# Kernel optimization log

Hardware: AMD Instinct MI355X
Metric: run time of the kernel (lower is better)

Reference implementation:

```python
import jax, jax.numpy as jnp
import numpy as np

T_SCALE = 160
NUM_SAMPLE = 32
FEAT_DIM = 2048
HIDDEN = 512
N_CLASS = 20
BATCH = 8


def build_sample_mask(tscale=T_SCALE, ns=NUM_SAMPLE):
    # Vectorized version of _get_interp1d_mask (prop_boundary_ratio=0, num_sample_perbin=1).
    # Returns mask of shape [tscale, ns, start, end] (already transposed as in the torch code).
    s = np.arange(tscale)[:, None, None]           # start
    e = np.arange(tscale)[None, :, None]           # end
    k = np.arange(ns)[None, None, :]
    pos = s + (e - s) * k / (ns - 1.0)             # [T, T, ns] sample positions
    Sg, Eg, Kg = np.broadcast_arrays(s, e, k)
    posf = pos.ravel(); Sf = Sg.ravel(); Ef = Eg.ravel(); Kf = Kg.ravel()
    valid = Ef >= Sf
    frac, dn = np.modf(posf)
    dn = dn.astype(np.int64)
    up = np.ceil(posf).astype(np.int64)
    mask = np.zeros((tscale, ns, tscale, tscale), dtype=np.float32)
    m1 = valid & (dn >= 0) & (dn <= tscale - 1)
    np.add.at(mask, (dn[m1], Kf[m1], Sf[m1], Ef[m1]), (1.0 - frac[m1]).astype(np.float32))
    m2 = valid & (up >= 0) & (up <= tscale - 1)
    np.add.at(mask, (up[m2], Kf[m2], Sf[m2], Ef[m2]), frac[m2].astype(np.float32))
    return jnp.asarray(mask)


def conv1d(x, w, padding):
    # x: [B, Cin, T], w: [Cout, Cin, K]
    return jax.lax.conv_general_dilated(
        x, w, window_strides=(1,), padding=[(padding, padding)],
        dimension_numbers=("NCH", "OIH", "NCH"))


def setup_inputs() -> dict:
    key = jax.random.key(0)
    ks = jax.random.split(key, 6)
    x = jax.random.normal(ks[0], (BATCH, T_SCALE, FEAT_DIM), dtype=jnp.float32)
    w1 = jax.random.normal(ks[1], (HIDDEN, FEAT_DIM, 3), dtype=jnp.float32) * 0.02
    b1 = jnp.zeros((HIDDEN,), dtype=jnp.float32)
    wc = jax.random.normal(ks[2], (N_CLASS, HIDDEN, 1), dtype=jnp.float32) * 0.05
    wa = jax.random.normal(ks[3], (1, HIDDEN, 3), dtype=jnp.float32) * 0.05
    ba = jnp.zeros((1,), dtype=jnp.float32)
    sample_mask = build_sample_mask()  # [T, ns, T, T]
    return {"x": x, "sample_mask": sample_mask, "w1": w1, "b1": b1,
            "wc": wc, "wa": wa, "ba": ba}


def reference(x, sample_mask, w1, b1, wc, wa, ba):
    ns = NUM_SAMPLE
    q = ns // 4  # 8
    xp = jnp.transpose(x, (0, 2, 1))                   # [B, F, T]
    feat = jax.nn.relu(conv1d(xp, w1, 1) + b1[None, :, None])   # [B, H, T] (dropout = eval/identity)
    y_class = conv1d(feat, wc, 0)                      # [B, C, T]
    y_atn = conv1d(feat, wa, 1) + ba[None, :, None]    # [B, 1, T]
    # boundary matching: matmul against sparse interpolation mask
    out = jnp.einsum("bct,tkij->bckij", y_class, sample_mask)   # [B, C, ns, T, T]
    out_start = out[:, :, :q].mean(axis=2)
    out_mid = out[:, :, q:ns - q].mean(axis=2)
    out_end = out[:, :, ns - q:].mean(axis=2)
    bmn_class = jnp.concatenate((out_start, out_mid, out_end), axis=1)  # [B, 3C, T, T]
    sig = jax.nn.sigmoid(y_atn)
    x_fg = (sig * feat).sum(-1, keepdims=True) / (sig.sum(-1, keepdims=True) + 1e-8)  # [B, H, 1]
    y_fg = jnp.einsum("oh,bht->bot", wc[:, :, 0], x_fg)  # conv_class 1x1, no bias
    return (y_class, y_fg, bmn_class)
```

## Files before the change

### kernel.cpp

```cpp
#include <hip/hip_runtime.h>
#include <math.h>

#define TS 160
#define FEATD 2048
#define HID 512
#define NC 20
#define NB 8
#define KZ 16

typedef __attribute__((ext_vector_type(8))) short bfrag;
typedef __attribute__((ext_vector_type(4))) float f32x4;

static __device__ __forceinline__ unsigned short f2bf(float f) {
  unsigned int u = __float_as_uint(f);
  unsigned int r = (u + 0x7FFFu + ((u >> 16) & 1u)) >> 16;
  return (unsigned short)r;
}
static __device__ __forceinline__ float bf2f(unsigned short s) {
  return __uint_as_float(((unsigned int)s) << 16);
}

static __device__ __forceinline__ void gload16(const void* g, void* l) {
  __builtin_amdgcn_global_load_lds((const __attribute__((address_space(1))) void*)g,
                                   (__attribute__((address_space(3))) void*)l, 16, 0, 0);
}

__global__ __launch_bounds__(256) void k_prep(const float* __restrict__ x,
                                              const float* __restrict__ w1,
                                              const float* __restrict__ ba,
                                              unsigned short* __restrict__ xb,
                                              unsigned short* __restrict__ wb,
                                              unsigned short* __restrict__ WT,
                                              float* __restrict__ y_atn) {
  __shared__ float Ls[FEATD * 3];
  const int tid = threadIdx.x;
  const int bx = blockIdx.x;
  if (bx < 1296) {
    const int idx = bx * 256 + tid;
    const int c = (idx & 255) * 8;
    const int row = idx >> 8;
    const int b = row / 162, pr = row - b * 162;
    unsigned short* o = xb + (size_t)row * FEATD + c;
    if (pr == 0 || pr == 161) {
      *(uint4*)o = make_uint4(0u, 0u, 0u, 0u);
    } else {
      const float* src = x + ((size_t)(b * TS + pr - 1)) * FEATD + c;
      float4 v0 = *(const float4*)src;
      float4 v1 = *(const float4*)(src + 4);
      unsigned short r[8] = {f2bf(v0.x), f2bf(v0.y), f2bf(v0.z), f2bf(v0.w),
                             f2bf(v1.x), f2bf(v1.y), f2bf(v1.z), f2bf(v1.w)};
      *(uint4*)o = *(const uint4*)r;
    }
  } else if (bx < 1808) {
    const int h = bx - 1296;
    const float4* src = (const float4*)(w1 + (size_t)h * (FEATD * 3));
    for (int e = tid; e < FEATD * 3 / 4; e += 256) ((float4*)Ls)[e] = src[e];
    __syncthreads();
    for (int oc = tid; oc < 768; oc += 256) {
      const int tap = oc >> 8;
      const int f0 = (oc & 255) * 8;
      unsigned short r[8];
      #pragma unroll
      for (int i = 0; i < 8; ++i) r[i] = f2bf(Ls[(f0 + i) * 3 + tap]);
      *(uint4*)&wb[((size_t)tap * HID + h) * FEATD + f0] = *(const uint4*)r;
    }
  } else if (bx < 2408) {
    const int idx = (bx - 1808) * 256 + tid;
    const int tau = idx % 160;
    const int dd = (idx / 160) % 320;
    const int g = idx / (160 * 320);
    float w = 0.f;
    if (dd >= 160) {
      const int d = dd - 160;
      const int k0 = (g == 0) ? 0 : (g == 1 ? 8 : 24);
      const int k1 = (g == 0) ? 8 : (g == 1 ? 24 : 32);
      for (int k = k0; k < k1; ++k) {
        float p = (float)(d * k) / 31.0f;
        float a = fabsf(p - (float)tau);
        w += fmaxf(0.f, 1.f - a);
      }
      w *= (g == 1) ? 0.0625f : 0.125f;
    }
    WT[idx] = f2bf(w);
  } else {
    const int idx = (bx - 2408) * 256 + tid;
    if (idx < NB * TS) y_atn[idx] = ba[0];
  }
}

__global__ __launch_bounds__(256, 2) void k_conv_mfma(const unsigned short* __restrict__ xb,
                                                      const unsigned short* __restrict__ wb,
                                                      unsigned short* __restrict__ part) {
  const int bb = blockIdx.x;
  const int hq = blockIdx.y;
  const int kz = blockIdx.z;
  const int tid = threadIdx.x;
  const int wid = tid >> 6, lane = tid & 63;

  __shared__ unsigned short Alds[162 * 64];
  __shared__ unsigned short Blds[3 * 128 * 64];

  const unsigned short* xbb = xb + (size_t)bb * 162 * FEATD;

  f32x4 acc[5][4] = {};
  const int wr = wid >> 1, wc = wid & 1;

  for (int s = 0; s < 2; ++s) {
    const int f0 = kz * 128 + s * 64;
    #pragma unroll
    for (int is = 0; is < 5; ++is) {
      const int ci = is * 256 + wid * 64 + lane;
      const int row = ci >> 3, c = ci & 7;
      gload16(xbb + (size_t)row * FEATD + f0 + ((c ^ (row & 7)) << 3),
              (char*)Alds + (size_t)(is * 256 + wid * 64) * 16);
    }
    #pragma unroll
    for (int is = 0; is < 12; ++is) {
      const int ci = is * 256 + wid * 64 + lane;
      const int tap = ci >> 10, rr = (ci >> 3) & 127, c = ci & 7;
      gload16(wb + ((size_t)(tap * HID + hq * 128 + rr)) * FEATD + f0 + ((c ^ (rr & 7)) << 3),
              (char*)Blds + (size_t)(is * 256 + wid * 64) * 16);
    }
    if (tid < 16) {
      const int row = 160 + (tid >> 3), c = tid & 7;
      uint4 v = *(const uint4*)(xbb + (size_t)row * FEATD + f0 + ((c ^ (row & 7)) << 3));
      *(uint4*)((char*)Alds + row * 128 + c * 16) = v;
    }
    __syncthreads();

    #pragma unroll
    for (int tap = 0; tap < 3; ++tap) {
      #pragma unroll
      for (int kk = 0; kk < 2; ++kk) {
        const int cc = kk * 4 + (lane >> 4);
        bfrag bfr[4];
        #pragma unroll
        for (int nf = 0; nf < 4; ++nf) {
          const int hh = wc * 64 + nf * 16 + (lane & 15);
          bfr[nf] = *(const bfrag*)((char*)Blds + (size_t)(((tap * 128 + hh) * 8) + (cc ^ (hh & 7))) * 16);
        }
        #pragma unroll
        for (int mi = 0; mi < 5; ++mi) {
          const int rr = wr * 80 + mi * 16 + (lane & 15) + tap;
          bfrag af = *(const bfrag*)((char*)Alds + (size_t)((rr * 8) + (cc ^ (rr & 7))) * 16);
          #pragma unroll
          for (int nf = 0; nf < 4; ++nf)
            acc[mi][nf] = __builtin_amdgcn_mfma_f32_16x16x32_bf16(af, bfr[nf], acc[mi][nf], 0, 0, 0);
        }
      }
    }
    __syncthreads();
  }

  unsigned short* pout = part + (size_t)kz * (NB * TS) * HID;
  #pragma unroll
  for (int mi = 0; mi < 5; ++mi) {
    const int r0 = bb * TS + wr * 80 + mi * 16 + (lane >> 4) * 4;
    #pragma unroll
    for (int nf = 0; nf < 4; ++nf) {
      const int c0 = hq * 128 + wc * 64 + nf * 16 + (lane & 15);
      #pragma unroll
      for (int i = 0; i < 4; ++i)
        pout[(size_t)(r0 + i) * HID + c0] = f2bf(acc[mi][nf][i]);
    }
  }
}

__global__ __launch_bounds__(256) void k_feat_head(const unsigned short* __restrict__ part,
                                                   const float* __restrict__ b1,
                                                   const float* __restrict__ wc,
                                                   const float* __restrict__ wa,
                                                   float* __restrict__ feat,
                                                   float* __restrict__ y_class,
                                                   float* __restrict__ y_atn) {
  const int bt = blockIdx.x;
  const int tid = threadIdx.x;
  __shared__ float fr[HID];
  __shared__ float sred[4][3];
  const int h0 = tid * 2;
  float a0 = b1[h0], a1 = b1[h0 + 1];
  #pragma unroll
  for (int kz = 0; kz < KZ; ++kz) {
    unsigned int v = *(const unsigned int*)&part[(size_t)kz * (NB * TS * HID) + (size_t)bt * HID + h0];
    a0 += bf2f((unsigned short)(v & 0xffff));
    a1 += bf2f((unsigned short)(v >> 16));
  }
  a0 = fmaxf(a0, 0.f);
  a1 = fmaxf(a1, 0.f);
  float2 fo; fo.x = a0; fo.y = a1;
  *(float2*)&feat[(size_t)bt * HID + h0] = fo;
  fr[h0] = a0; fr[h0 + 1] = a1;
  float s0 = a0 * wa[h0 * 3 + 0] + a1 * wa[h0 * 3 + 3];
  float s1 = a0 * wa[h0 * 3 + 1] + a1 * wa[h0 * 3 + 4];
  float s2 = a0 * wa[h0 * 3 + 2] + a1 * wa[h0 * 3 + 5];
  #pragma unroll
  for (int off = 32; off; off >>= 1) {
    s0 += __shfl_xor(s0, off);
    s1 += __shfl_xor(s1, off);
    s2 += __shfl_xor(s2, off);
  }
  const int wv = tid >> 6, lane = tid & 63;
  if (lane == 0) { sred[wv][0] = s0; sred[wv][1] = s1; sred[wv][2] = s2; }
  __syncthreads();
  const int b = bt / TS, t = bt - b * TS;
  for (int c = wv; c < NC; c += 4) {
    float p = 0.f;
    #pragma unroll
    for (int i2 = 0; i2 < 8; ++i2) p += fr[lane + 64 * i2] * wc[c * HID + lane + 64 * i2];
    #pragma unroll
    for (int off = 32; off; off >>= 1) p += __shfl_xor(p, off);
    if (lane == 0) y_class[((size_t)b * NC + c) * TS + t] = p;
  }
  if (tid == 0) {
    float S0 = sred[0][0] + sred[1][0] + sred[2][0] + sred[3][0];
    float S1 = sred[0][1] + sred[1][1] + sred[2][1] + sred[3][1];
    float S2 = sred[0][2] + sred[1][2] + sred[2][2] + sred[3][2];
    atomicAdd(&y_atn[bt], S1);
    if (t < TS - 1) atomicAdd(&y_atn[bt + 1], S0);
    if (t > 0)      atomicAdd(&y_atn[bt - 1], S2);
  }
}

__global__ __launch_bounds__(256) void k_tail(const float* __restrict__ y_class,
                                              const unsigned short* __restrict__ WT,
                                              const float* __restrict__ feat,
                                              const float* __restrict__ y_atn,
                                              const float* __restrict__ wc,
                                              float* __restrict__ y_fg,
                                              float* __restrict__ bmn) {
  __shared__ char Tlds[64000 + 65536];
  const int tid = threadIdx.x;

  if (blockIdx.y == 3) {
    if (blockIdx.x >= NB) return;
    const int b = blockIdx.x;
    float* sig = (float*)Tlds;
    float* red = sig + TS;
    float* xfg = red + 8;
    float s = 0.f;
    if (tid < TS) { s = 1.f / (1.f + expf(-y_atn[b * TS + tid])); sig[tid] = s; }
    float r = s;
    #pragma unroll
    for (int off = 32; off; off >>= 1) r += __shfl_xor(r, off);
    if ((tid & 63) == 0) red[tid >> 6] = r;
    __syncthreads();
    const float inv = 1.f / (red[0] + red[1] + red[2] + red[3] + 1e-8f);
    for (int h = tid; h < HID; h += 256) {
      float a = 0.f;
      for (int t = 0; t < TS; ++t) a += sig[t] * feat[((size_t)b * TS + t) * HID + h];
      xfg[h] = a * inv;
    }
    __syncthreads();
    const int wv = tid >> 6, lane = tid & 63;
    for (int c = wv; c < NC; c += 4) {
      float p = 0.f;
      #pragma unroll
      for (int i2 = 0; i2 < 8; ++i2) {
        int h = lane + 64 * i2;
        p += wc[c * HID + h] * xfg[h];
      }
      #pragma unroll
      for (int off = 32; off; off >>= 1) p += __shfl_xor(p, off);
      if (lane == 0) y_fg[b * NC + c] = p;
    }
    return;
  }

  char* Alds = Tlds;
  char* Wlds = Tlds + 64000;
  const int i = blockIdx.x;
  const int g = blockIdx.y;
  const int wid = tid >> 6, lane = tid & 63;

  const char* wtb = (const char*)WT + (size_t)g * 102400 + (size_t)(160 - i) * 320;
  #pragma unroll
  for (int it = 0; it < 16; ++it) {
    const int idx = it * 256 + tid;
    int row = idx / 25, c = idx - row * 25;
    if (row > 159) row = 159;
    if (c > 19) c = 0;
    gload16(wtb + (size_t)row * 320 + c * 16, Wlds + (size_t)idx * 16);
  }
  for (int e = 0; e < 13; ++e) {
    const int ci = e * 256 + tid;
    if (ci < 3200) {
      const int row = ci / 20, c = ci - row * 20;
      const int tb = i + c * 8;
      const float* yr = y_class + (size_t)row * TS;
      unsigned short r8[8];
      #pragma unroll
      for (int k = 0; k < 8; ++k) {
        const int t = tb + k;
        r8[k] = (t < TS) ? f2bf(yr[t]) : (unsigned short)0;
      }
      *(uint4*)(Alds + (size_t)row * 400 + c * 16) = *(const uint4*)r8;
    }
  }
  __syncthreads();

  const int wr = wid >> 1, wcq = wid & 1;
  f32x4 acc[5][5] = {};

  #pragma unroll
  for (int ks = 0; ks < 5; ++ks) {
    const int cc = ks * 4 + (lane >> 4);
    bfrag bfr[5];
    #pragma unroll
    for (int nf = 0; nf < 5; ++nf) {
      const int j = wcq * 80 + nf * 16 + (lane & 15);
      bfr[nf] = *(const bfrag*)(Wlds + (size_t)j * 400 + cc * 16);
    }
    #pragma unroll
    for (int mf = 0; mf < 5; ++mf) {
      const int r = wr * 80 + mf * 16 + (lane & 15);
      bfrag af = *(const bfrag*)(Alds + (size_t)r * 400 + cc * 16);
      #pragma unroll
      for (int nf = 0; nf < 5; ++nf)
        acc[mf][nf] = __builtin_amdgcn_mfma_f32_16x16x32_bf16(af, bfr[nf], acc[mf][nf], 0, 0, 0);
    }
  }

  #pragma unroll
  for (int mf = 0; mf < 5; ++mf) {
    const int r0 = wr * 80 + mf * 16 + (lane >> 4) * 4;
    #pragma unroll
    for (int reg = 0; reg < 4; ++reg) {
      const int r = r0 + reg;
      const int b = r / 20, c = r - b * 20;
      float* base = bmn + (((size_t)(b * 60 + g * 20 + c) * TS) + i) * TS;
      #pragma unroll
      for (int nf = 0; nf < 5; ++nf) {
        const int j = wcq * 80 + nf * 16 + (lane & 15);
        base[j] = acc[mf][nf][reg];
      }
    }
  }
}

extern "C" void kernel_launch(void* const* d_in, const int* in_sizes, int n_in,
                              void* d_out, int out_size, void* d_ws, size_t ws_size,
                              hipStream_t stream) {
  const float* x  = (const float*)d_in[0];
  const float* w1 = (const float*)d_in[2];
  const float* b1 = (const float*)d_in[3];
  const float* wc = (const float*)d_in[4];
  const float* wa = (const float*)d_in[5];
  const float* ba = (const float*)d_in[6];

  float* out     = (float*)d_out;
  float* y_class = out;
  float* y_fg    = out + NB * NC * TS;
  float* bmn     = out + NB * NC * TS + NB * NC;

  unsigned short* part = (unsigned short*)d_ws;
  float* feat  = (float*)((char*)d_ws + (size_t)KZ * NB * TS * HID * 2);
  float* y_atn = feat + NB * TS * HID;
  unsigned short* xb = (unsigned short*)(y_atn + 2048);
  unsigned short* wb = xb + (size_t)NB * 162 * FEATD;
  unsigned short* WT = wb + (size_t)3 * HID * FEATD;

  k_prep<<<2413, 256, 0, stream>>>(x, w1, ba, xb, wb, WT, y_atn);
  k_conv_mfma<<<dim3(8, 4, KZ), 256, 0, stream>>>(xb, wb, part);
  k_feat_head<<<NB * TS, 256, 0, stream>>>(part, b1, wc, wa, feat, y_class, y_atn);
  k_tail<<<dim3(160, 4), 256, 0, stream>>>(y_class, WT, feat, y_atn, wc, y_fg, bmn);
}
```

Before: 72.38 us.

## Double-buffer conv LDS stages, halve split-K, batch feat_head rows per block

The conv kernel now splits K over 8 chunks instead of 16, so each block handles 256 features in four 64-wide stages. Those stages are double-buffered in LDS so the next stage's global-to-LDS loads are issued while the current one runs MFMAs. The A-tile padding rows are loaded by clamping the row index instead of a separate scalar path. The feat_head kernel processes 4 time rows per block, which reuses the bias and wa loads and cuts the partial-sum reads by half. The trade-off is twice the LDS per conv block, occupancy dropping to one block per CU, and 256 conv blocks where there were 512.

```diff
diff --git a/kernel.cpp b/kernel.cpp
--- a/kernel.cpp
+++ b/kernel.cpp
@@ -6,7 +6,7 @@
 #define HID 512
 #define NC 20
 #define NB 8
-#define KZ 16
+#define KZ 8
 
 typedef __attribute__((ext_vector_type(8))) short bfrag;
 typedef __attribute__((ext_vector_type(4))) float f32x4;
@@ -88,7 +88,7 @@
   }
 }
 
-__global__ __launch_bounds__(256, 2) void k_conv_mfma(const unsigned short* __restrict__ xb,
+__global__ __launch_bounds__(256, 1) void k_conv_mfma(const unsigned short* __restrict__ xb,
                                                       const unsigned short* __restrict__ wb,
                                                       unsigned short* __restrict__ part) {
   const int bb = blockIdx.x;
@@ -97,37 +97,40 @@
   const int tid = threadIdx.x;
   const int wid = tid >> 6, lane = tid & 63;
 
-  __shared__ unsigned short Alds[162 * 64];
-  __shared__ unsigned short Blds[3 * 128 * 64];
+  __shared__ unsigned short Alds[2][12288];
+  __shared__ unsigned short Blds[2][24576];
 
   const unsigned short* xbb = xb + (size_t)bb * 162 * FEATD;
 
   f32x4 acc[5][4] = {};
   const int wr = wid >> 1, wc = wid & 1;
 
-  for (int s = 0; s < 2; ++s) {
-    const int f0 = kz * 128 + s * 64;
-    #pragma unroll
-    for (int is = 0; is < 5; ++is) {
+  auto STAGE = [&](int half, int s) {
+    const int f0 = kz * 256 + s * 64;
+    #pragma unroll
+    for (int is = 0; is < 6; ++is) {
       const int ci = is * 256 + wid * 64 + lane;
-      const int row = ci >> 3, c = ci & 7;
+      int row = ci >> 3;
+      if (row > 161) row = 161;
+      const int c = ci & 7;
       gload16(xbb + (size_t)row * FEATD + f0 + ((c ^ (row & 7)) << 3),
-              (char*)Alds + (size_t)(is * 256 + wid * 64) * 16);
+              (char*)Alds[half] + (size_t)(is * 256 + wid * 64) * 16);
     }
     #pragma unroll
     for (int is = 0; is < 12; ++is) {
       const int ci = is * 256 + wid * 64 + lane;
       const int tap = ci >> 10, rr = (ci >> 3) & 127, c = ci & 7;
       gload16(wb + ((size_t)(tap * HID + hq * 128 + rr)) * FEATD + f0 + ((c ^ (rr & 7)) << 3),
-              (char*)Blds + (size_t)(is * 256 + wid * 64) * 16);
-    }
-    if (tid < 16) {
-      const int row = 160 + (tid >> 3), c = tid & 7;
-      uint4 v = *(const uint4*)(xbb + (size_t)row * FEATD + f0 + ((c ^ (row & 7)) << 3));
-      *(uint4*)((char*)Alds + row * 128 + c * 16) = v;
-    }
-    __syncthreads();
-
+              (char*)Blds[half] + (size_t)(is * 256 + wid * 64) * 16);
+    }
+  };
+
+  STAGE(0, 0);
+  __syncthreads();
+
+  int cur = 0;
+  for (int s = 0; s < 4; ++s) {
+    if (s < 3) STAGE(cur ^ 1, s + 1);
     #pragma unroll
     for (int tap = 0; tap < 3; ++tap) {
       #pragma unroll
@@ -137,12 +140,12 @@
         #pragma unroll
         for (int nf = 0; nf < 4; ++nf) {
           const int hh = wc * 64 + nf * 16 + (lane & 15);
-          bfr[nf] = *(const bfrag*)((char*)Blds + (size_t)(((tap * 128 + hh) * 8) + (cc ^ (hh & 7))) * 16);
+          bfr[nf] = *(const bfrag*)((char*)Blds[cur] + (size_t)(((tap * 128 + hh) * 8) + (cc ^ (hh & 7))) * 16);
         }
         #pragma unroll
         for (int mi = 0; mi < 5; ++mi) {
           const int rr = wr * 80 + mi * 16 + (lane & 15) + tap;
-          bfrag af = *(const bfrag*)((char*)Alds + (size_t)((rr * 8) + (cc ^ (rr & 7))) * 16);
+          bfrag af = *(const bfrag*)((char*)Alds[cur] + (size_t)((rr * 8) + (cc ^ (rr & 7))) * 16);
           #pragma unroll
           for (int nf = 0; nf < 4; ++nf)
             acc[mi][nf] = __builtin_amdgcn_mfma_f32_16x16x32_bf16(af, bfr[nf], acc[mi][nf], 0, 0, 0);
@@ -150,6 +153,7 @@
       }
     }
     __syncthreads();
+    cur ^= 1;
   }
 
   unsigned short* pout = part + (size_t)kz * (NB * TS) * HID;
@@ -173,48 +177,63 @@
                                                    float* __restrict__ feat,
                                                    float* __restrict__ y_class,
                                                    float* __restrict__ y_atn) {
-  const int bt = blockIdx.x;
+  const int r0 = blockIdx.x * 4;
   const int tid = threadIdx.x;
-  __shared__ float fr[HID];
-  __shared__ float sred[4][3];
+  const int wv = tid >> 6, lane = tid & 63;
+  __shared__ float fr[4][HID];
+  __shared__ float sred[4][4][3];
   const int h0 = tid * 2;
-  float a0 = b1[h0], a1 = b1[h0 + 1];
-  #pragma unroll
-  for (int kz = 0; kz < KZ; ++kz) {
-    unsigned int v = *(const unsigned int*)&part[(size_t)kz * (NB * TS * HID) + (size_t)bt * HID + h0];
-    a0 += bf2f((unsigned short)(v & 0xffff));
-    a1 += bf2f((unsigned short)(v >> 16));
-  }
-  a0 = fmaxf(a0, 0.f);
-  a1 = fmaxf(a1, 0.f);
-  float2 fo; fo.x = a0; fo.y = a1;
-  *(float2*)&feat[(size_t)bt * HID + h0] = fo;
-  fr[h0] = a0; fr[h0 + 1] = a1;
-  float s0 = a0 * wa[h0 * 3 + 0] + a1 * wa[h0 * 3 + 3];
-  float s1 = a0 * wa[h0 * 3 + 1] + a1 * wa[h0 * 3 + 4];
-  float s2 = a0 * wa[h0 * 3 + 2] + a1 * wa[h0 * 3 + 5];
-  #pragma unroll
-  for (int off = 32; off; off >>= 1) {
-    s0 += __shfl_xor(s0, off);
-    s1 += __shfl_xor(s1, off);
-    s2 += __shfl_xor(s2, off);
-  }
-  const int wv = tid >> 6, lane = tid & 63;
-  if (lane == 0) { sred[wv][0] = s0; sred[wv][1] = s1; sred[wv][2] = s2; }
+  const float bb0 = b1[h0], bb1 = b1[h0 + 1];
+  const float wa0 = wa[h0 * 3 + 0], wa1 = wa[h0 * 3 + 1], wa2 = wa[h0 * 3 + 2];
+  const float wa3 = wa[h0 * 3 + 3], wa4 = wa[h0 * 3 + 4], wa5 = wa[h0 * 3 + 5];
+
+  #pragma unroll
+  for (int r = 0; r < 4; ++r) {
+    const int bt = r0 + r;
+    float a0 = bb0, a1 = bb1;
+    #pragma unroll
+    for (int kz = 0; kz < KZ; ++kz) {
+      unsigned int v = *(const unsigned int*)&part[(size_t)kz * (NB * TS * HID) + (size_t)bt * HID + h0];
+      a0 += bf2f((unsigned short)(v & 0xffff));
+      a1 += bf2f((unsigned short)(v >> 16));
+    }
+    a0 = fmaxf(a0, 0.f);
+    a1 = fmaxf(a1, 0.f);
+    float2 fo; fo.x = a0; fo.y = a1;
+    *(float2*)&feat[(size_t)bt * HID + h0] = fo;
+    fr[r][h0] = a0; fr[r][h0 + 1] = a1;
+    float s0 = a0 * wa0 + a1 * wa3;
+    float s1 = a0 * wa1 + a1 * wa4;
+    float s2 = a0 * wa2 + a1 * wa5;
+    #pragma unroll
+    for (int off = 32; off; off >>= 1) {
+      s0 += __shfl_xor(s0, off);
+      s1 += __shfl_xor(s1, off);
+      s2 += __shfl_xor(s2, off);
+    }
+    if (lane == 0) { sred[r][wv][0] = s0; sred[r][wv][1] = s1; sred[r][wv][2] = s2; }
+  }
   __syncthreads();
-  const int b = bt / TS, t = bt - b * TS;
-  for (int c = wv; c < NC; c += 4) {
-    float p = 0.f;
-    #pragma unroll
-    for (int i2 = 0; i2 < 8; ++i2) p += fr[lane + 64 * i2] * wc[c * HID + lane + 64 * i2];
-    #pragma unroll
-    for (int off = 32; off; off >>= 1) p += __shfl_xor(p, off);
-    if (lane == 0) y_class[((size_t)b * NC + c) * TS + t] = p;
-  }
-  if (tid == 0) {
-    float S0 = sred[0][0] + sred[1][0] + sred[2][0] + sred[3][0];
-    float S1 = sred[0][1] + sred[1][1] + sred[2][1] + sred[3][1];
-    float S2 = sred[0][2] + sred[1][2] + sred[2][2] + sred[3][2];
+
+  #pragma unroll
+  for (int r = 0; r < 4; ++r) {
+    const int bt = r0 + r;
+    const int b = bt / TS, t = bt - b * TS;
+    for (int c = wv; c < NC; c += 4) {
+      float p = 0.f;
+      #pragma unroll
+      for (int i2 = 0; i2 < 8; ++i2) p += fr[r][lane + 64 * i2] * wc[c * HID + lane + 64 * i2];
+      #pragma unroll
+      for (int off = 32; off; off >>= 1) p += __shfl_xor(p, off);
+      if (lane == 0) y_class[((size_t)b * NC + c) * TS + t] = p;
+    }
+  }
+  if (tid < 4) {
+    const int bt = r0 + tid;
+    const int t = bt % TS;
+    float S0 = sred[tid][0][0] + sred[tid][1][0] + sred[tid][2][0] + sred[tid][3][0];
+    float S1 = sred[tid][0][1] + sred[tid][1][1] + sred[tid][2][1] + sred[tid][3][1];
+    float S2 = sred[tid][0][2] + sred[tid][1][2] + sred[tid][2][2] + sred[tid][3][2];
     atomicAdd(&y_atn[bt], S1);
     if (t < TS - 1) atomicAdd(&y_atn[bt + 1], S0);
     if (t > 0)      atomicAdd(&y_atn[bt - 1], S2);
@@ -361,6 +380,6 @@
 
   k_prep<<<2413, 256, 0, stream>>>(x, w1, ba, xb, wb, WT, y_atn);
   k_conv_mfma<<<dim3(8, 4, KZ), 256, 0, stream>>>(xb, wb, part);
-  k_feat_head<<<NB * TS, 256, 0, stream>>>(part, b1, wc, wa, feat, y_class, y_atn);
+  k_feat_head<<<NB * TS / 4, 256, 0, stream>>>(part, b1, wc, wa, feat, y_class, y_atn);
   k_tail<<<dim3(160, 4), 256, 0, stream>>>(y_class, WT, feat, y_atn, wc, y_fg, bmn);
 }
```

Result: slower. 78.72 us (+8.8%).
